# Performance work log

Measured on AMD Instinct MI355X. Metric: run time of the kernel, lower is better.

Reference implementation:

```python
import jax, jax.numpy as jnp
import numpy as np

D_MODEL = 1024
POOL = 2048
K = 16
D_FF = 4096
N_HEADS = 16
TEMP = 1.0
EPS = 1e-5


def _ln(x, g, b):
    mu = jnp.mean(x, axis=-1, keepdims=True)
    var = jnp.mean((x - mu) ** 2, axis=-1, keepdims=True)
    return (x - mu) * jax.lax.rsqrt(var + EPS) * g + b


def setup_inputs() -> dict:
    key = jax.random.key(0)
    ks = jax.random.split(key, 12)
    s = 0.02
    return {
        "x": jax.random.normal(ks[0], (4, 1024, D_MODEL), jnp.float32),
        "w_router": s * jax.random.normal(ks[1], (D_MODEL, POOL), jnp.float32),
        "b_router": jnp.zeros((POOL,), jnp.float32),
        "firing": s * jax.random.normal(ks[2], (POOL, D_FF), jnp.float32),
        "w_pool_out": s * jax.random.normal(ks[3], (D_FF, D_MODEL), jnp.float32),
        "b_pool_out": jnp.zeros((D_MODEL,), jnp.float32),
        "w_in": s * jax.random.normal(ks[4], (D_MODEL, 3 * D_MODEL), jnp.float32),
        "b_in": jnp.zeros((3 * D_MODEL,), jnp.float32),
        "w_attn_out": s * jax.random.normal(ks[5], (D_MODEL, D_MODEL), jnp.float32),
        "b_attn_out": jnp.zeros((D_MODEL,), jnp.float32),
        "g1": jnp.ones((D_MODEL,), jnp.float32),
        "beta1": jnp.zeros((D_MODEL,), jnp.float32),
        "g2": jnp.ones((D_MODEL,), jnp.float32),
        "beta2": jnp.zeros((D_MODEL,), jnp.float32),
    }


def reference(x, w_router, b_router, firing, w_pool_out, b_pool_out,
              w_in, b_in, w_attn_out, b_attn_out, g1, beta1, g2, beta2):
    B, S, D = x.shape
    Hd = D // N_HEADS
    # --- Context router: score every neuron, select top-k, softmax weights ---
    scores = x @ w_router + b_router                      # [B,S,P]
    top_vals, top_idx = jax.lax.top_k(scores, K)          # [B,S,K]
    weights = jax.nn.softmax(top_vals / TEMP, axis=-1)    # [B,S,K]
    # --- Neuron pool: gather firing patterns, weighted combine, GELU, project ---
    patterns = firing[top_idx]                            # [B,S,K,d_ff] gather
    combined = jnp.einsum('bsk,bskf->bsf', weights, patterns)  # [B,S,d_ff]
    neuron_out = jax.nn.gelu(combined, approximate=False) @ w_pool_out + b_pool_out  # [B,S,D]
    # --- Self-attention over neuron_out (dropout inactive at eval) ---
    qkv = neuron_out @ w_in + b_in                        # [B,S,3D]
    q, k, v = jnp.split(qkv, 3, axis=-1)
    q = q.reshape(B, S, N_HEADS, Hd).transpose(0, 2, 1, 3)
    k = k.reshape(B, S, N_HEADS, Hd).transpose(0, 2, 1, 3)
    v = v.reshape(B, S, N_HEADS, Hd).transpose(0, 2, 1, 3)
    logits = jnp.einsum('bhqd,bhkd->bhqk', q, k) / jnp.sqrt(jnp.float32(Hd))
    probs = jax.nn.softmax(logits, axis=-1)
    ctx = jnp.einsum('bhqk,bhkd->bhqd', probs, v)
    ctx = ctx.transpose(0, 2, 1, 3).reshape(B, S, D)
    attn_out = ctx @ w_attn_out + b_attn_out
    # --- Residuals + norms ---
    h = _ln(x + attn_out, g1, beta1)
    out = _ln(h + neuron_out, g2, beta2)
    return out
```

## Files before the change

### kernel.cpp

```cpp
#include <hip/hip_runtime.h>
#include <math.h>

typedef __attribute__((ext_vector_type(8))) __bf16 bf16x8;
typedef __attribute__((ext_vector_type(4))) __bf16 bf16x4;
typedef __attribute__((ext_vector_type(4))) float f32x4;

#define DEV static __device__ __forceinline__

DEV float b2f(unsigned short u){ union{unsigned i; float f;} c; c.i=((unsigned)u)<<16; return c.f; }
DEV unsigned short f2b(float f){
  union{float f; unsigned u;} c; c.f=f;
  unsigned r = 0x7FFFu + ((c.u>>16)&1u);
  return (unsigned short)((c.u + r)>>16);
}
DEV unsigned pack2(float a, float b){ return (unsigned)f2b(a) | ((unsigned)f2b(b)<<16); }
DEV float gelu_exact(float x){ return 0.5f*x*(1.f+erff(x*0.70710678118654752f)); }

typedef __attribute__((address_space(1))) void gas_void;
typedef __attribute__((address_space(3))) void las_void;
DEV void gload_lds16(const unsigned short* g, unsigned short* l){
  __builtin_amdgcn_global_load_lds((const gas_void*)g, (las_void*)l, 16, 0, 0);
}

template<int N> DEV void waitcnt_vm(){
  if constexpr(N==0) asm volatile("s_waitcnt vmcnt(0)" ::: "memory");
  else if constexpr(N==2) asm volatile("s_waitcnt vmcnt(2)" ::: "memory");
  else if constexpr(N==3) asm volatile("s_waitcnt vmcnt(3)" ::: "memory");
  else if constexpr(N==4) asm volatile("s_waitcnt vmcnt(4)" ::: "memory");
  else                    asm volatile("s_waitcnt vmcnt(0)" ::: "memory");
}

__global__ __launch_bounds__(256) void k_cast_bf16(const float* __restrict__ in,
                                                   unsigned short* __restrict__ out, long n4)
{
  long i = (long)blockIdx.x*256 + threadIdx.x;
  if (i >= n4) return;
  float4 v = ((const float4*)in)[i];
  ushort4 o; o.x=f2b(v.x); o.y=f2b(v.y); o.z=f2b(v.z); o.w=f2b(v.w);
  ((ushort4*)out)[i] = o;
}

__global__ __launch_bounds__(256) void k_transpose_cast(const float* __restrict__ in,
                                                        unsigned short* __restrict__ out,
                                                        int R, int C)
{
  __shared__ float tile[32][33];
  int tc = blockIdx.x*32, tr = blockIdx.y*32;
  int lx = threadIdx.x & 31, ly = threadIdx.x >> 5;
  #pragma unroll
  for (int s=0;s<4;s++) tile[ly+s*8][lx] = in[(long)(tr+ly+s*8)*C + tc+lx];
  __syncthreads();
  #pragma unroll
  for (int s=0;s<4;s++) out[(long)(tc+ly+s*8)*R + tr+lx] = f2b(tile[lx][ly+s*8]);
}

template<int FM, int FN, int OMODE>
__global__ __launch_bounds__(256) void k_gemm_bt(
  const unsigned short* __restrict__ A, long lda, long sAb,
  const unsigned short* __restrict__ Bt, long ldb, long sBb,
  float* __restrict__ Cf, unsigned short* __restrict__ Cb, long ldc, long sCb,
  const float* __restrict__ bias, int Kiters)
{
  constexpr int BM = 32*FM, BN = 32*FN;
  constexpr int AR16 = BM/16, TOT16 = (BM+BN)/16;
  constexpr int UNITS = TOT16/4;
  static_assert(TOT16 % 4 == 0, "stage units must split across 4 waves");
  __shared__ __align__(16) unsigned short S[3][TOT16*512];
  const int tid = threadIdx.x;
  const int wave = tid>>6, lane = tid&63;
  const int wr = wave>>1, wc = wave&1;
  const int l15 = lane&15, lhi = lane>>4;
  const int lrow = lane>>2;
  const int lcol = ((lane&3) ^ (lrow&3))*8;

  const int gx = gridDim.x;
  const int nwg = gx*gridDim.y;
  const int id = blockIdx.y*gx + blockIdx.x;
  const int sid = (id&7)*(nwg>>3) + (id>>3);
  const long bm = (long)(sid / gx)*BM, bn = (long)(sid % gx)*BN;

  const unsigned short* Ab  = A  + (long)blockIdx.z*sAb + bm*lda;
  const unsigned short* Btb = Bt + (long)blockIdx.z*sBb + bn*ldb;

  f32x4 acc[FM][FN];
  #pragma unroll
  for (int i=0;i<FM;i++)
    #pragma unroll
    for (int j=0;j<FN;j++) acc[i][j] = (f32x4){0.f,0.f,0.f,0.f};

  auto STAGE = [&](int kt, int buf){
    const long k0 = (long)kt*32;
    #pragma unroll
    for (int u=0; u<UNITS; ++u) {
      const int t = wave + u*4;
      const unsigned short* g;
      if (t < AR16) g = Ab  + (long)(t*16 + lrow)*lda + k0 + lcol;
      else          g = Btb + (long)((t-AR16)*16 + lrow)*ldb + k0 + lcol;
      gload_lds16(g, &S[buf][t*512]);
    }
  };
  auto COMPUTE = [&](int buf){
    const unsigned short* Sb = S[buf];
    bf16x8 af[FM], bfr[FN];
    #pragma unroll
    for (int i=0;i<FM;i++) {
      const int r = wr*(BM/2) + i*16 + l15;
      af[i]  = *(const bf16x8*)&Sb[r*32 + ((lhi ^ (r&3))*8)];
    }
    #pragma unroll
    for (int j=0;j<FN;j++) {
      const int r = wc*(BN/2) + j*16 + l15;
      bfr[j] = *(const bf16x8*)&Sb[BM*32 + r*32 + ((lhi ^ (r&3))*8)];
    }
    #pragma unroll
    for (int i=0;i<FM;i++)
      #pragma unroll
      for (int j=0;j<FN;j++)
        acc[i][j] = __builtin_amdgcn_mfma_f32_16x16x32_bf16(af[i], bfr[j], acc[i][j], 0,0,0);
  };

  STAGE(0, 0);
  if (Kiters > 1) STAGE(1, 1);
  for (int kt=0; kt<Kiters; ++kt) {
    if (kt+1 < Kiters) waitcnt_vm<UNITS>();
    else               waitcnt_vm<0>();
    __builtin_amdgcn_s_barrier();
    __builtin_amdgcn_sched_barrier(0);
    COMPUTE(kt%3);
    if (kt+2 < Kiters) STAGE(kt+2, (kt+2)%3);
  }

  #pragma unroll
  for (int i=0;i<FM;i++) {
    #pragma unroll
    for (int j=0;j<FN;j++) {
      long col = bn + wc*(BN/2) + j*16 + l15;
      float bb = bias ? bias[col] : 0.f;
      #pragma unroll
      for (int q=0;q<4;q++) {
        long row = bm + wr*(BM/2) + i*16 + lhi*4 + q;
        float v = acc[i][j][q] + bb;
        long off = (long)blockIdx.z*sCb + row*ldc + col;
        if constexpr (OMODE==0 || OMODE==2) Cf[off] = v;
        if constexpr (OMODE==1 || OMODE==2) Cb[off] = f2b(v);
      }
    }
  }
}

__global__ __launch_bounds__(256) void k_topk_softmax(const float* __restrict__ scores,
                                                      int* __restrict__ topidx,
                                                      float* __restrict__ topw)
{
  __shared__ float sv[2048];
  __shared__ float rv[256];
  __shared__ int   ri[256];
  __shared__ float selv[16];
  __shared__ int   seli[16];
  const int tid = threadIdx.x;
  const long t = blockIdx.x;
  const float* row = scores + t*2048;
  #pragma unroll
  for (int s=0;s<2;s++) ((float4*)sv)[tid + s*256] = ((const float4*)row)[tid + s*256];
  __syncthreads();
  for (int it=0; it<16; ++it) {
    float best = -1e30f; int bidx = 0x7FFFFFFF;
    #pragma unroll
    for (int s=0;s<8;s++) {
      int j = tid + s*256;
      float v = sv[j];
      if (v > best) { best = v; bidx = j; }
    }
    rv[tid]=best; ri[tid]=bidx;
    __syncthreads();
    if (tid < 64) {
      float bv = rv[tid]; int bi = ri[tid];
      #pragma unroll
      for (int s=1;s<4;s++) {
        float v2 = rv[tid+64*s]; int i2 = ri[tid+64*s];
        if (v2 > bv || (v2 == bv && i2 < bi)) { bv=v2; bi=i2; }
      }
      #pragma unroll
      for (int off=32; off; off>>=1) {
        float v2 = __shfl_xor(bv, off); int i2 = __shfl_xor(bi, off);
        if (v2 > bv || (v2 == bv && i2 < bi)) { bv=v2; bi=i2; }
      }
      if (tid == 0) { selv[it]=bv; seli[it]=bi; sv[bi] = -1e30f; }
    }
    __syncthreads();
  }
  if (tid == 0) {
    float m = selv[0], ssum = 0.f, w[16];
    #pragma unroll
    for (int k2=0;k2<16;k2++){ w[k2] = expf(selv[k2]-m); ssum += w[k2]; }
    float inv = 1.f/ssum;
    #pragma unroll
    for (int k2=0;k2<16;k2++){ topw[t*16+k2]=w[k2]*inv; topidx[t*16+k2]=seli[k2]; }
  }
}

__global__ __launch_bounds__(256) void k_gather_gelu(const int* __restrict__ topidx,
                                                     const float* __restrict__ topw,
                                                     const unsigned short* __restrict__ firing,
                                                     unsigned short* __restrict__ gact)
{
  __shared__ int idx[4][16]; __shared__ float w[4][16];
  const int tid = threadIdx.x;
  const int c = blockIdx.x & 7;
  const long t0 = (long)(blockIdx.x >> 3) * 4;
  if (tid < 64) {
    int tok = tid >> 4, k = tid & 15;
    idx[tok][k] = topidx[(t0+tok)*16 + k];
    w[tok][k]   = topw[(t0+tok)*16 + k];
  }
  __syncthreads();
  const int tok = tid >> 6, lane = tid & 63;
  const int f0 = c*512 + lane*8;
  float acc[8] = {0,0,0,0,0,0,0,0};
  #pragma unroll
  for (int k=0;k<16;k++) {
    uint4 v = *(const uint4*)(firing + (long)idx[tok][k]*4096 + f0);
    const unsigned short* pu = (const unsigned short*)&v;
    float wk = w[tok][k];
    #pragma unroll
    for (int e=0;e<8;e++) acc[e] += wk * b2f(pu[e]);
  }
  float g[8];
  #pragma unroll
  for (int e=0;e<8;e++) g[e] = gelu_exact(acc[e]);
  uint4 ov;
  ov.x = pack2(g[0],g[1]); ov.y = pack2(g[2],g[3]);
  ov.z = pack2(g[4],g[5]); ov.w = pack2(g[6],g[7]);
  *(uint4*)(gact + (t0+tok)*4096 + f0) = ov;
}

__global__ __launch_bounds__(256) void k_vtrans(const unsigned short* __restrict__ qkv,
                                                unsigned short* __restrict__ vT)
{
  __shared__ unsigned short tile[64][65];
  int bh = blockIdx.y; int b = bh>>4, h = bh&15;
  long t0 = (long)blockIdx.x*64;
  const int tid = threadIdx.x;
  #pragma unroll
  for (int s=0;s<16;s++) {
    int i = tid + s*256;
    int r = i>>6, c = i&63;
    tile[r][c] = qkv[ (long)(b*1024 + t0 + r)*3072 + 2048 + h*64 + c ];
  }
  __syncthreads();
  #pragma unroll
  for (int s=0;s<16;s++) {
    int i = tid + s*256;
    int c = i>>6, r = i&63;
    vT[ (long)bh*65536 + (long)c*1024 + t0 + r ] = tile[r][c];
  }
}

__global__ __launch_bounds__(256) void k_flash_attn(
  const unsigned short* __restrict__ qkv,
  const unsigned short* __restrict__ vT,
  unsigned short* __restrict__ ctx)
{
  __shared__ __align__(16) unsigned short Qs[128*64];
  __shared__ __align__(16) unsigned short Ks[2][128*64];
  __shared__ __align__(16) unsigned short Vs[2][64*128];
  const int tid = threadIdx.x;
  const int wave = tid>>6, lane = tid&63;
  const int l15 = lane&15, lhi = lane>>4;
  const int bh = blockIdx.y, b = bh>>4, h = bh&15;
  const long q0 = (long)blockIdx.x*128;
  const unsigned short* Qg = qkv + ((long)b*1024 + q0)*3072 + h*64;
  const unsigned short* Kg = qkv + (long)b*1024*3072 + 1024 + h*64;
  const unsigned short* Vg = vT + (long)bh*65536;

  {
    const int sr = lane>>3, sc = (lane&7)^sr;
    #pragma unroll
    for (int uu=0; uu<4; ++uu){
      int u = wave + uu*4;
      gload_lds16(Qg + (long)(u*8+sr)*3072 + sc*8, &Qs[u*512]);
    }
  }
  auto STAGE_KV = [&](int t, int s){
    const long kv0 = (long)t*128;
    const int sr = lane>>3, sc = (lane&7)^sr;
    #pragma unroll
    for (int uu=0; uu<4; ++uu){
      int u = wave + uu*4;
      gload_lds16(Kg + (kv0 + u*8 + sr)*3072 + sc*8, &Ks[s][u*512]);
    }
    const int vc = (lane&15) ^ ((wave&1)*4 + lhi);
    #pragma unroll
    for (int uu=0; uu<4; ++uu){
      int u = wave + uu*4;
      gload_lds16(Vg + (long)(u*4+lhi)*1024 + kv0 + vc*8, &Vs[s][u*512]);
    }
  };

  STAGE_KV(0, 0);
  __syncthreads();

  bf16x8 qf[2][2];
  #pragma unroll
  for (int jq=0;jq<2;jq++){
    const int r = wave*32 + jq*16 + l15;
    #pragma unroll
    for (int ks=0;ks<2;ks++)
      qf[jq][ks] = *(const bf16x8*)&Qs[r*64 + (((ks*4+lhi)^(r&7))*8)];
  }

  f32x4 acco[2][4];
  #pragma unroll
  for (int mi=0;mi<2;mi++)
    #pragma unroll
    for (int nf=0;nf<4;nf++) acco[mi][nf] = (f32x4){0.f,0.f,0.f,0.f};
  float m_run[2] = {-1e30f,-1e30f}, l_run[2] = {0.f,0.f};

  int sel = 0;
  for (int t=0; t<8; ++t) {
    if (t < 7) STAGE_KV(t+1, sel^1);
    f32x4 accs[8][2];
    #pragma unroll
    for (int fk=0;fk<8;fk++){
      accs[fk][0] = (f32x4){0.f,0.f,0.f,0.f};
      accs[fk][1] = (f32x4){0.f,0.f,0.f,0.f};
      const int r = fk*16 + l15;
      bf16x8 k0 = *(const bf16x8*)&Ks[sel][r*64 + ((lhi^(r&7))*8)];
      accs[fk][0] = __builtin_amdgcn_mfma_f32_16x16x32_bf16(k0, qf[0][0], accs[fk][0],0,0,0);
      accs[fk][1] = __builtin_amdgcn_mfma_f32_16x16x32_bf16(k0, qf[1][0], accs[fk][1],0,0,0);
      bf16x8 k1 = *(const bf16x8*)&Ks[sel][r*64 + (((4+lhi)^(r&7))*8)];
      accs[fk][0] = __builtin_amdgcn_mfma_f32_16x16x32_bf16(k1, qf[0][1], accs[fk][0],0,0,0);
      accs[fk][1] = __builtin_amdgcn_mfma_f32_16x16x32_bf16(k1, qf[1][1], accs[fk][1],0,0,0);
    }
    bf16x8 pa[2][4];
    float fsc[2];
    #pragma unroll
    for (int jq=0;jq<2;jq++){
      float mt = -1e30f;
      #pragma unroll
      for (int fk=0;fk<8;fk++)
        #pragma unroll
        for (int q=0;q<4;q++) mt = fmaxf(mt, accs[fk][jq][q]);
      mt = fmaxf(mt, __shfl_xor(mt,16));
      mt = fmaxf(mt, __shfl_xor(mt,32));
      mt *= 0.125f;
      float mnew = fmaxf(m_run[jq], mt);
      float fj = __expf(m_run[jq] - mnew);
      float ssum = 0.f;
      #pragma unroll
      for (int fk=0;fk<8;fk++)
        #pragma unroll
        for (int q=0;q<4;q++){
          float p = __expf(accs[fk][jq][q]*0.125f - mnew);
          ssum += p;
          pa[jq][fk>>1][(fk&1)*4+q] = (__bf16)p;
        }
      ssum += __shfl_xor(ssum,16);
      ssum += __shfl_xor(ssum,32);
      l_run[jq] = l_run[jq]*fj + ssum;
      m_run[jq] = mnew;
      fsc[jq] = fj;
    }
    #pragma unroll
    for (int mi=0;mi<2;mi++)
      #pragma unroll
      for (int q=0;q<4;q++){
        float fr = __shfl(fsc[mi], (lane&48)|(lhi*4+q));
        #pragma unroll
        for (int nf=0;nf<4;nf++) acco[mi][nf][q] *= fr;
      }
    #pragma unroll
    for (int kk=0;kk<4;kk++)
      #pragma unroll
      for (int nf=0;nf<4;nf++){
        const int rv = nf*16 + l15;
        const int cb = kk*4 + (lhi>>1);
        bf16x4 v0 = *(const bf16x4*)&Vs[sel][rv*128 + (( cb   ^(l15&7))*8) + (lhi&1)*4];
        bf16x4 v1 = *(const bf16x4*)&Vs[sel][rv*128 + (((cb+2)^(l15&7))*8) + (lhi&1)*4];
        bf16x8 vb = __builtin_shufflevector(v0, v1, 0,1,2,3,4,5,6,7);
        acco[0][nf] = __builtin_amdgcn_mfma_f32_16x16x32_bf16(pa[0][kk], vb, acco[0][nf],0,0,0);
        acco[1][nf] = __builtin_amdgcn_mfma_f32_16x16x32_bf16(pa[1][kk], vb, acco[1][nf],0,0,0);
      }
    __syncthreads();
    sel ^= 1;
  }

  #pragma unroll
  for (int mi=0;mi<2;mi++)
    #pragma unroll
    for (int q=0;q<4;q++){
      float lr = __shfl(l_run[mi], (lane&48)|(lhi*4+q));
      float inv = 1.f/lr;
      long row = q0 + wave*32 + mi*16 + lhi*4 + q;
      #pragma unroll
      for (int nf=0;nf<4;nf++)
        ctx[((long)b*1024 + row)*1024 + h*64 + nf*16 + l15] = f2b(acco[mi][nf][q]*inv);
    }
}

__global__ __launch_bounds__(256) void k_ln_res(const float* __restrict__ a,
                                                const float* b,
                                                const float* __restrict__ g,
                                                const float* __restrict__ be,
                                                float* out)
{
  const long t = blockIdx.x;
  const int tid = threadIdx.x;
  const int wave = tid>>6, lane = tid&63;
  float4 av = ((const float4*)(a + t*1024))[tid];
  float4 bv = ((const float4*)(b + t*1024))[tid];
  float4 sv = {av.x+bv.x, av.y+bv.y, av.z+bv.z, av.w+bv.w};
  float sum = sv.x+sv.y+sv.z+sv.w;
  float sq  = sv.x*sv.x + sv.y*sv.y + sv.z*sv.z + sv.w*sv.w;
  #pragma unroll
  for (int off=32; off; off>>=1){ sum += __shfl_xor(sum,off); sq += __shfl_xor(sq,off); }
  __shared__ float s1[4], s2[4];
  if (lane==0){ s1[wave]=sum; s2[wave]=sq; }
  __syncthreads();
  sum = s1[0]+s1[1]+s1[2]+s1[3];
  sq  = s2[0]+s2[1]+s2[2]+s2[3];
  float mu  = sum * (1.f/1024.f);
  float var = sq * (1.f/1024.f) - mu*mu;
  float rs  = rsqrtf(var + 1e-5f);
  float4 gv  = ((const float4*)g)[tid];
  float4 bev = ((const float4*)be)[tid];
  float4 ov = { (sv.x-mu)*rs*gv.x + bev.x,
                (sv.y-mu)*rs*gv.y + bev.y,
                (sv.z-mu)*rs*gv.z + bev.z,
                (sv.w-mu)*rs*gv.w + bev.w };
  ((float4*)(out + t*1024))[tid] = ov;
}

extern "C" void kernel_launch(void* const* d_in, const int* in_sizes, int n_in,
                              void* d_out, int out_size, void* d_ws, size_t ws_size,
                              hipStream_t stream)
{
  const float* x        = (const float*)d_in[0];
  const float* w_router = (const float*)d_in[1];
  const float* b_router = (const float*)d_in[2];
  const float* firing   = (const float*)d_in[3];
  const float* w_pool   = (const float*)d_in[4];
  const float* b_pool   = (const float*)d_in[5];
  const float* w_in     = (const float*)d_in[6];
  const float* b_in     = (const float*)d_in[7];
  const float* w_ao     = (const float*)d_in[8];
  const float* b_ao     = (const float*)d_in[9];
  const float* g1       = (const float*)d_in[10];
  const float* be1      = (const float*)d_in[11];
  const float* g2       = (const float*)d_in[12];
  const float* be2      = (const float*)d_in[13];
  float* out = (float*)d_out;
  char* ws = (char*)d_ws;

  unsigned short* xb    = (unsigned short*)(ws + 0);
  unsigned short* wrT   = (unsigned short*)(ws + 8388608);
  unsigned short* firb  = (unsigned short*)(ws + 12582912);
  unsigned short* wpoT  = (unsigned short*)(ws + 29360128);
  unsigned short* winT  = (unsigned short*)(ws + 37748736);
  unsigned short* waoT  = (unsigned short*)(ws + 44040192);
  float*  scores        = (float*)(ws + 46137344);
  unsigned short* gact  = (unsigned short*)(ws + 46137344);
  int*    topi          = (int*)(ws + 79691776);
  float*  topw          = (float*)(ws + 79953920);
  float*  neuf          = (float*)(ws + 80216064);
  unsigned short* neub  = (unsigned short*)(ws + 96993280);
  unsigned short* qkvb  = (unsigned short*)(ws + 105381888);
  unsigned short* vT    = (unsigned short*)(ws + 130547712);
  unsigned short* ctx   = (unsigned short*)(ws + 138936320);
  float*  attn          = (float*)(ws + 147324928);

  if (ws_size < 164102144u) return;

  k_cast_bf16<<<4096, 256, 0, stream>>>(x, xb, 4096L*1024/4);
  k_cast_bf16<<<8192, 256, 0, stream>>>(firing, firb, 2048L*4096/4);
  k_transpose_cast<<<dim3(2048/32, 1024/32), 256, 0, stream>>>(w_router, wrT, 1024, 2048);
  k_transpose_cast<<<dim3(1024/32, 4096/32), 256, 0, stream>>>(w_pool,   wpoT, 4096, 1024);
  k_transpose_cast<<<dim3(3072/32, 1024/32), 256, 0, stream>>>(w_in,     winT, 1024, 3072);
  k_transpose_cast<<<dim3(1024/32, 1024/32), 256, 0, stream>>>(w_ao,     waoT, 1024, 1024);

  k_gemm_bt<4,4,0><<<dim3(16,32,1),256,0,stream>>>(xb,1024,0, wrT,1024,0,
        scores,nullptr,2048,0, b_router, 32);
  k_topk_softmax<<<4096,256,0,stream>>>(scores, topi, topw);
  k_gather_gelu<<<8192,256,0,stream>>>(topi, topw, firb, gact);

  k_gemm_bt<4,2,2><<<dim3(16,32,1),256,0,stream>>>(gact,4096,0, wpoT,4096,0,
        neuf,neub,1024,0, b_pool, 128);

  k_gemm_bt<4,4,1><<<dim3(24,32,1),256,0,stream>>>(neub,1024,0, winT,1024,0,
        nullptr,qkvb,3072,0, b_in, 32);

  k_vtrans<<<dim3(16,64),256,0,stream>>>(qkvb, vT);
  k_flash_attn<<<dim3(8,64),256,0,stream>>>(qkvb, vT, ctx);

  k_gemm_bt<4,2,0><<<dim3(16,32,1),256,0,stream>>>(ctx,1024,0, waoT,1024,0,
        attn,nullptr,1024,0, b_ao, 32);

  k_ln_res<<<4096,256,0,stream>>>(x, attn, g1, be1, attn);
  k_ln_res<<<4096,256,0,stream>>>(attn, neuf, g2, be2, out);
}
```

Before: 307.1 us.

## Generalize GEMM wave layout and enlarge per-wave tiles for more reuse

Templates the bf16 GEMM kernel on its wave grid (WR x WC) and makes each wave compute an 8x4 grid of 16x16 MFMA fragments instead of 2x2 or 2x1. All four GEMMs get larger block tiles: 256x128 with four waves, or 128x128 with two waves for the narrow-N GEMMs. The compute loop now loads one A fragment at a time to keep register pressure down, and launch bounds ask for two blocks per CU. Larger tiles raise the MFMA work per LDS and global load, but they mean fewer blocks, so occupancy and wave-level parallelism drop and register use per wave goes up.

```diff
diff --git a/kernel.cpp b/kernel.cpp
--- a/kernel.cpp
+++ b/kernel.cpp
@@ -23,10 +23,12 @@
 }
 
 template<int N> DEV void waitcnt_vm(){
-  if constexpr(N==0) asm volatile("s_waitcnt vmcnt(0)" ::: "memory");
+  if constexpr(N==0)      asm volatile("s_waitcnt vmcnt(0)" ::: "memory");
   else if constexpr(N==2) asm volatile("s_waitcnt vmcnt(2)" ::: "memory");
   else if constexpr(N==3) asm volatile("s_waitcnt vmcnt(3)" ::: "memory");
   else if constexpr(N==4) asm volatile("s_waitcnt vmcnt(4)" ::: "memory");
+  else if constexpr(N==6) asm volatile("s_waitcnt vmcnt(6)" ::: "memory");
+  else if constexpr(N==8) asm volatile("s_waitcnt vmcnt(8)" ::: "memory");
   else                    asm volatile("s_waitcnt vmcnt(0)" ::: "memory");
 }
 
@@ -54,21 +56,22 @@
   for (int s=0;s<4;s++) out[(long)(tc+ly+s*8)*R + tr+lx] = f2b(tile[lx][ly+s*8]);
 }
 
-template<int FM, int FN, int OMODE>
-__global__ __launch_bounds__(256) void k_gemm_bt(
+template<int WR, int WC, int FM, int FN, int OMODE>
+__global__ __launch_bounds__(WR*WC*64, 2) void k_gemm_bt(
   const unsigned short* __restrict__ A, long lda, long sAb,
   const unsigned short* __restrict__ Bt, long ldb, long sBb,
   float* __restrict__ Cf, unsigned short* __restrict__ Cb, long ldc, long sCb,
   const float* __restrict__ bias, int Kiters)
 {
-  constexpr int BM = 32*FM, BN = 32*FN;
+  constexpr int WAVES = WR*WC;
+  constexpr int BM = WR*FM*16, BN = WC*FN*16;
   constexpr int AR16 = BM/16, TOT16 = (BM+BN)/16;
-  constexpr int UNITS = TOT16/4;
-  static_assert(TOT16 % 4 == 0, "stage units must split across 4 waves");
+  constexpr int UNITS = TOT16/WAVES;
+  static_assert(TOT16 % WAVES == 0, "stage units must split across waves");
   __shared__ __align__(16) unsigned short S[3][TOT16*512];
   const int tid = threadIdx.x;
   const int wave = tid>>6, lane = tid&63;
-  const int wr = wave>>1, wc = wave&1;
+  const int wr = wave/WC, wc = wave%WC;
   const int l15 = lane&15, lhi = lane>>4;
   const int lrow = lane>>2;
   const int lcol = ((lane&3) ^ (lrow&3))*8;
@@ -92,7 +95,7 @@
     const long k0 = (long)kt*32;
     #pragma unroll
     for (int u=0; u<UNITS; ++u) {
-      const int t = wave + u*4;
+      const int t = wave + u*WAVES;
       const unsigned short* g;
       if (t < AR16) g = Ab  + (long)(t*16 + lrow)*lda + k0 + lcol;
       else          g = Btb + (long)((t-AR16)*16 + lrow)*ldb + k0 + lcol;
@@ -101,22 +104,20 @@
   };
   auto COMPUTE = [&](int buf){
     const unsigned short* Sb = S[buf];
-    bf16x8 af[FM], bfr[FN];
+    bf16x8 bfr[FN];
+    #pragma unroll
+    for (int j=0;j<FN;j++) {
+      const int r = wc*(FN*16) + j*16 + l15;
+      bfr[j] = *(const bf16x8*)&Sb[BM*32 + r*32 + ((lhi ^ (r&3))*8)];
+    }
     #pragma unroll
     for (int i=0;i<FM;i++) {
-      const int r = wr*(BM/2) + i*16 + l15;
-      af[i]  = *(const bf16x8*)&Sb[r*32 + ((lhi ^ (r&3))*8)];
-    }
-    #pragma unroll
-    for (int j=0;j<FN;j++) {
-      const int r = wc*(BN/2) + j*16 + l15;
-      bfr[j] = *(const bf16x8*)&Sb[BM*32 + r*32 + ((lhi ^ (r&3))*8)];
-    }
-    #pragma unroll
-    for (int i=0;i<FM;i++)
+      const int r = wr*(FM*16) + i*16 + l15;
+      bf16x8 a = *(const bf16x8*)&Sb[r*32 + ((lhi ^ (r&3))*8)];
       #pragma unroll
       for (int j=0;j<FN;j++)
-        acc[i][j] = __builtin_amdgcn_mfma_f32_16x16x32_bf16(af[i], bfr[j], acc[i][j], 0,0,0);
+        acc[i][j] = __builtin_amdgcn_mfma_f32_16x16x32_bf16(a, bfr[j], acc[i][j], 0,0,0);
+    }
   };
 
   STAGE(0, 0);
@@ -134,11 +135,11 @@
   for (int i=0;i<FM;i++) {
     #pragma unroll
     for (int j=0;j<FN;j++) {
-      long col = bn + wc*(BN/2) + j*16 + l15;
+      long col = bn + wc*(FN*16) + j*16 + l15;
       float bb = bias ? bias[col] : 0.f;
       #pragma unroll
       for (int q=0;q<4;q++) {
-        long row = bm + wr*(BM/2) + i*16 + lhi*4 + q;
+        long row = bm + wr*(FM*16) + i*16 + lhi*4 + q;
         float v = acc[i][j][q] + bb;
         long off = (long)blockIdx.z*sCb + row*ldc + col;
         if constexpr (OMODE==0 || OMODE==2) Cf[off] = v;
@@ -478,21 +479,21 @@
   k_transpose_cast<<<dim3(3072/32, 1024/32), 256, 0, stream>>>(w_in,     winT, 1024, 3072);
   k_transpose_cast<<<dim3(1024/32, 1024/32), 256, 0, stream>>>(w_ao,     waoT, 1024, 1024);
 
-  k_gemm_bt<4,4,0><<<dim3(16,32,1),256,0,stream>>>(xb,1024,0, wrT,1024,0,
+  k_gemm_bt<2,2,8,4,0><<<dim3(16,16,1),256,0,stream>>>(xb,1024,0, wrT,1024,0,
         scores,nullptr,2048,0, b_router, 32);
   k_topk_softmax<<<4096,256,0,stream>>>(scores, topi, topw);
   k_gather_gelu<<<8192,256,0,stream>>>(topi, topw, firb, gact);
 
-  k_gemm_bt<4,2,2><<<dim3(16,32,1),256,0,stream>>>(gact,4096,0, wpoT,4096,0,
+  k_gemm_bt<1,2,8,4,2><<<dim3(8,32,1),128,0,stream>>>(gact,4096,0, wpoT,4096,0,
         neuf,neub,1024,0, b_pool, 128);
 
-  k_gemm_bt<4,4,1><<<dim3(24,32,1),256,0,stream>>>(neub,1024,0, winT,1024,0,
+  k_gemm_bt<2,2,8,4,1><<<dim3(24,16,1),256,0,stream>>>(neub,1024,0, winT,1024,0,
         nullptr,qkvb,3072,0, b_in, 32);
 
   k_vtrans<<<dim3(16,64),256,0,stream>>>(qkvb, vT);
   k_flash_attn<<<dim3(8,64),256,0,stream>>>(qkvb, vT, ctx);
 
-  k_gemm_bt<4,2,0><<<dim3(16,32,1),256,0,stream>>>(ctx,1024,0, waoT,1024,0,
+  k_gemm_bt<1,2,8,4,0><<<dim3(8,32,1),128,0,stream>>>(ctx,1024,0, waoT,1024,0,
         attn,nullptr,1024,0, b_ao, 32);
 
   k_ln_res<<<4096,256,0,stream>>>(x, attn, g1, be1, attn);
```

Measured after the change: 340.5 us. 10.9% more time.
